# Kernel tuning notes

Measured on AMD Instinct MI355X. Metric: run time of the kernel, lower is better.

The kernel has to match this reference:

```python
import jax, jax.numpy as jnp
import numpy as np

B, TD, TE, H, D, V = 64, 256, 256, 512, 256, 50000

def setup_inputs() -> dict:
    key = jax.random.key(0)
    ks = jax.random.split(key, 8)
    return {
        "enc_outputs": jax.random.normal(ks[0], (B, TE, H), jnp.float32),
        "dec_inputs": jax.random.randint(ks[1], (B, TD), 0, V, jnp.int32),
        "state_h": jax.random.normal(ks[2], (B, H), jnp.float32),
        "state_c": jax.random.normal(ks[3], (B, H), jnp.float32),
        "E": jax.random.normal(ks[4], (V, D), jnp.float32) * 0.02,
        "W": jax.random.normal(ks[5], (D, 4 * H), jnp.float32) * 0.02,
        "U": jax.random.normal(ks[6], (H, 4 * H), jnp.float32) * 0.02,
        "b": jnp.zeros((4 * H,), jnp.float32),
    }


def _masked_lstm(x, mask, h0, c0, W, U, b):
    """Keras-semantics masked LSTM: at masked steps states AND outputs are
    carried from the previous step. Gate order i, f, g(cell), o."""
    def step(carry, inp):
        h, c = carry
        xt, mt = inp  # xt: [B,D], mt: [B]
        z = xt @ W + h @ U + b  # [B,4H]
        i, f, g, o = jnp.split(z, 4, axis=-1)
        c_new = jax.nn.sigmoid(f) * c + jax.nn.sigmoid(i) * jnp.tanh(g)
        h_new = jax.nn.sigmoid(o) * jnp.tanh(c_new)
        m = mt[:, None]
        h2 = jnp.where(m, h_new, h)
        c2 = jnp.where(m, c_new, c)
        return (h2, c2), h2
    xs = (jnp.swapaxes(x, 0, 1), jnp.swapaxes(mask, 0, 1))  # time-major
    (hT, cT), hs = jax.lax.scan(step, (h0, c0), xs)
    return jnp.swapaxes(hs, 0, 1), hT, cT  # [B,Td,H]


def reference(enc_outputs, dec_inputs, state_h, state_c, E, W, U, b):
    mask = dec_inputs != 0  # mask_zero=True on Embedding
    x = E[dec_inputs]  # [B,Td,D]
    dec_outputs, hT, cT = _masked_lstm(x, mask, state_h, state_c, W, U, b)
    # Keras Attention (Luong dot, no scale): query=dec_outputs, key=value=enc_outputs
    scores = jnp.einsum('bqh,bkh->bqk', dec_outputs, enc_outputs)
    probs = jax.nn.softmax(scores, axis=-1)
    ctx = jnp.einsum('bqk,bkh->bqh', probs, enc_outputs)
    # query mask propagated from embedding zeroes masked query rows
    ctx = jnp.where(mask[..., None], ctx, 0.0)
    return (ctx, hT, cT)
```

## Files before the change

### kernel.cpp

```cpp
#include <hip/hip_runtime.h>
#include <stdint.h>

typedef __attribute__((ext_vector_type(4))) float f32x4;
typedef __attribute__((ext_vector_type(4))) int i32x4;
typedef __attribute__((ext_vector_type(4))) unsigned short u16x4;
typedef __attribute__((ext_vector_type(8))) __bf16 bf16x8;

#define NB 64
#define TD 256
#define TE 256
#define HH 512
#define DD 256
#define FH 2048
#define KT 768
#define LDK 776

#define WS_ENC   0u
#define WS_ENCT  16777216u
#define WS_DEC   33554432u
#define WS_HPING 50331648u
#define WS_FLAGS 50462720u
#define WS_WT    50528256u

#define OUT_HT 8388608u
#define OUT_CT 8421376u

__device__ inline unsigned short f2b(float f) {
  union { float f; unsigned u; } x; x.f = f;
  unsigned r = x.u + 0x7FFFu + ((x.u >> 16) & 1u);
  return (unsigned short)(r >> 16);
}
__device__ inline float sigm(float x)   { return 1.0f / (1.0f + __expf(-x)); }
__device__ inline float tanhf_(float x) { return 1.0f - 2.0f / (__expf(2.0f * x) + 1.0f); }

__device__ inline f32x4 mfma_bf16(i32x4 a, i32x4 b, f32x4 c) {
  return __builtin_amdgcn_mfma_f32_16x16x32_bf16(
      __builtin_bit_cast(bf16x8, a), __builtin_bit_cast(bf16x8, b), c, 0, 0, 0);
}

__device__ inline unsigned poll_flag(const unsigned* p) {
  unsigned v;
  asm volatile("global_load_dword %0, %1, off sc0 sc1\n\ts_waitcnt vmcnt(0)"
               : "=v"(v) : "v"(p) : "memory");
  return v;
}
__device__ inline i32x4 load4_bypass(const void* p) {
  i32x4 v;
  asm volatile("global_load_dwordx4 %0, %1, off sc0 sc1" : "=v"(v) : "v"(p) : "memory");
  return v;
}
__device__ inline void store_u16_wt(unsigned short* p, unsigned v) {
  asm volatile("global_store_short %0, %1, off sc0 sc1" :: "v"(p), "v"(v) : "memory");
}
__device__ inline void vm_drain() {
  asm volatile("s_waitcnt vmcnt(0)" ::: "memory");
}
__device__ inline void store_flag(unsigned* p, unsigned v) {
  asm volatile("global_store_dword %0, %1, off sc0 sc1" :: "v"(p), "v"(v) : "memory");
}

__global__ __launch_bounds__(256) void enc_prep(const float* __restrict__ enc,
                                                unsigned short* __restrict__ enc_bf,
                                                unsigned short* __restrict__ encT_bf) {
  __shared__ float tile[64][65];
  const int bid = blockIdx.x;
  const int b  = bid >> 5;
  const int kt = (bid >> 3) & 3;
  const int ht = bid & 7;
  const int tr = threadIdx.x >> 6;
  const int tc = threadIdx.x & 63;
#pragma unroll
  for (int i = 0; i < 16; ++i) {
    const int ke = i * 4 + tr;
    const float v = enc[((size_t)b * TE + kt * 64 + ke) * HH + ht * 64 + tc];
    enc_bf[((size_t)b * TE + kt * 64 + ke) * HH + ht * 64 + tc] = f2b(v);
    tile[ke][tc] = v;
  }
  __syncthreads();
  const int hr4 = threadIdx.x >> 4;
  const int k4  = (threadIdx.x & 15) * 4;
#pragma unroll
  for (int jr = 0; jr < 4; ++jr) {
    const int hr = jr * 16 + hr4;
    u16x4 p = { f2b(tile[k4 + 0][hr]), f2b(tile[k4 + 1][hr]),
                f2b(tile[k4 + 2][hr]), f2b(tile[k4 + 3][hr]) };
    *(u16x4*)&encT_bf[((size_t)b * HH + ht * 64 + hr) * TE + kt * 64 + k4] = p;
  }
}

__global__ __launch_bounds__(256) void w_prep(const float* __restrict__ W,
                                              const float* __restrict__ U,
                                              unsigned short* __restrict__ wT) {
  __shared__ float tile[64][65];
  const int kt = blockIdx.x >> 5;
  const int ct = blockIdx.x & 31;
  const int tr = threadIdx.x >> 6;
  const int tc = threadIdx.x & 63;
#pragma unroll
  for (int i = 0; i < 16; ++i) {
    const int kr = i * 4 + tr;
    const int k  = kt * 64 + kr;
    const float v = (k < DD) ? W[(size_t)k * FH + ct * 64 + tc]
                             : U[(size_t)(k - DD) * FH + ct * 64 + tc];
    tile[kr][tc] = v;
  }
  __syncthreads();
  const int cr4 = threadIdx.x >> 4;
  const int k4  = (threadIdx.x & 15) * 4;
#pragma unroll
  for (int jr = 0; jr < 4; ++jr) {
    const int cr = jr * 16 + cr4;
    u16x4 p = { f2b(tile[k4 + 0][cr]), f2b(tile[k4 + 1][cr]),
                f2b(tile[k4 + 2][cr]), f2b(tile[k4 + 3][cr]) };
    *(u16x4*)&wT[((size_t)ct * 64 + cr) * KT + kt * 64 + k4] = p;
  }
}

__global__ __launch_bounds__(256) void h0_prep(const float* __restrict__ h0,
                                               unsigned short* __restrict__ h_ping,
                                               unsigned* __restrict__ flags) {
  const int i = blockIdx.x * 256 + threadIdx.x;
  if (i < NB * HH) h_ping[i] = f2b(h0[i]);
  if (i < 2 * TD * 32) flags[i] = 0u;
}

__global__ __launch_bounds__(64, 1) void lstm_kernel(
    const float* __restrict__ E, const int* __restrict__ ids,
    const float* __restrict__ h0f, const float* __restrict__ c0f,
    const unsigned short* __restrict__ wT, const float* __restrict__ bias,
    unsigned short* __restrict__ h_ping,
    unsigned short* __restrict__ dec_bf,
    float* __restrict__ out,
    unsigned* __restrict__ flags)
{
  const int lane = threadIdx.x;
  const int g  = blockIdx.x >> 5;
  const int s  = blockIdx.x & 31;
  const int u0 = s << 4;
  const int lhi = lane >> 4;
  const int llo = lane & 15;

  __shared__ __align__(16) unsigned short wt[64 * LDK];
  __shared__ int ids_l[32][260];

  {
    const int r = lane;
    const int c = (r >> 4) * 512 + u0 + (r & 15);
    const unsigned short* src = wT + (size_t)c * KT;
#pragma unroll 8
    for (int j = 0; j < 96; ++j)
      *(i32x4*)&wt[r * LDK + j * 8] = *(const i32x4*)(src + j * 8);
  }
  for (int idx = lane; idx < 32 * 256; idx += 64) {
    const int row = idx >> 8, tt = idx & 255;
    ids_l[row][tt] = ids[(g * 32 + row) * TD + tt];
  }
  __syncthreads();

  float bb[4];
#pragma unroll
  for (int gg = 0; gg < 4; ++gg) bb[gg] = bias[gg * 512 + u0 + llo];

  float h_reg[2][4], c_reg[2][4];
#pragma unroll
  for (int mt = 0; mt < 2; ++mt)
#pragma unroll
    for (int r = 0; r < 4; ++r) {
      const int b = g * 32 + mt * 16 + lhi * 4 + r;
      h_reg[mt][r] = h0f[b * HH + u0 + llo];
      c_reg[mt][r] = c0f[b * HH + u0 + llo];
    }

  unsigned short* hp0 = h_ping;
  unsigned short* hp1 = h_ping + NB * HH;

  for (int t = 0; t < TD; ++t) {
    const unsigned short* h_src = (t & 1) ? hp1 : hp0;
    unsigned short*       h_dst = (t & 1) ? hp0 : hp1;

    int xid[2], mid[2][4];
#pragma unroll
    for (int mt = 0; mt < 2; ++mt) {
      xid[mt] = ids_l[mt * 16 + llo][t];
#pragma unroll
      for (int r = 0; r < 4; ++r) mid[mt][r] = ids_l[mt * 16 + lhi * 4 + r][t];
    }

    i32x4 xf[2][8];
#pragma unroll
    for (int mt = 0; mt < 2; ++mt)
#pragma unroll
      for (int kk = 0; kk < 8; ++kk) {
        const float* ep = E + (size_t)xid[mt] * DD + kk * 32 + lhi * 8;
        f32x4 lo = *(const f32x4*)ep;
        f32x4 hi = *(const f32x4*)(ep + 4);
        union { i32x4 i; unsigned short sh[8]; } u;
        u.sh[0] = f2b(lo[0]); u.sh[1] = f2b(lo[1]); u.sh[2] = f2b(lo[2]); u.sh[3] = f2b(lo[3]);
        u.sh[4] = f2b(hi[0]); u.sh[5] = f2b(hi[1]); u.sh[6] = f2b(hi[2]); u.sh[7] = f2b(hi[3]);
        xf[mt][kk] = u.i;
      }

    f32x4 acc[2][4];
#pragma unroll
    for (int mt = 0; mt < 2; ++mt)
#pragma unroll
      for (int gg = 0; gg < 4; ++gg) acc[mt][gg] = (f32x4){0.f, 0.f, 0.f, 0.f};
#pragma unroll
    for (int kk = 0; kk < 8; ++kk) {
      const int ko = kk * 32 + lhi * 8;
#pragma unroll
      for (int gg = 0; gg < 4; ++gg) {
        i32x4 bfr = *(const i32x4*)&wt[(gg * 16 + llo) * LDK + ko];
        acc[0][gg] = mfma_bf16(xf[0][kk], bfr, acc[0][gg]);
        acc[1][gg] = mfma_bf16(xf[1][kk], bfr, acc[1][gg]);
      }
    }

    if (t > 0) {
      const unsigned* f = flags + ((size_t)g * TD + (t - 1)) * 32;
      for (;;) {
        unsigned v = (lane < 32) ? poll_flag(f + lane) : 1u;
        if (__all(v != 0)) break;
        __builtin_amdgcn_s_sleep(1);
      }
    }

    {
      const unsigned short* hb0 = h_src + (size_t)(g * 32 + llo) * HH + lhi * 8;
      const unsigned short* hb1 = hb0 + 16 * HH;
      i32x4 ha0[16], ha1[16];
#pragma unroll
      for (int kk = 0; kk < 16; ++kk) {
        ha0[kk] = load4_bypass(hb0 + kk * 32);
        ha1[kk] = load4_bypass(hb1 + kk * 32);
      }
      vm_drain();
      __builtin_amdgcn_sched_barrier(0);
#pragma unroll
      for (int kk = 0; kk < 16; ++kk) {
        const int ko = DD + kk * 32 + lhi * 8;
#pragma unroll
        for (int gg = 0; gg < 4; ++gg) {
          i32x4 bfr = *(const i32x4*)&wt[(gg * 16 + llo) * LDK + ko];
          acc[0][gg] = mfma_bf16(ha0[kk], bfr, acc[0][gg]);
          acc[1][gg] = mfma_bf16(ha1[kk], bfr, acc[1][gg]);
        }
      }
    }

    unsigned hb_out[2][4];
#pragma unroll
    for (int mt = 0; mt < 2; ++mt) {
#pragma unroll
      for (int r = 0; r < 4; ++r) {
        const float zi = acc[mt][0][r] + bb[0];
        const float zf = acc[mt][1][r] + bb[1];
        const float zg = acc[mt][2][r] + bb[2];
        const float zo = acc[mt][3][r] + bb[3];
        const float cn = sigm(zf) * c_reg[mt][r] + sigm(zi) * tanhf_(zg);
        const float hn = sigm(zo) * tanhf_(cn);
        if (mid[mt][r] != 0) { c_reg[mt][r] = cn; h_reg[mt][r] = hn; }
        hb_out[mt][r] = f2b(h_reg[mt][r]);
      }
    }

    if (t < TD - 1) {
#pragma unroll
      for (int mt = 0; mt < 2; ++mt)
#pragma unroll
        for (int r = 0; r < 4; ++r) {
          const int b = g * 32 + mt * 16 + lhi * 4 + r;
          store_u16_wt(h_dst + (size_t)b * HH + u0 + llo, hb_out[mt][r]);
        }
      vm_drain();
      if (lane == 0)
        store_flag(flags + ((size_t)g * TD + t) * 32 + s, 1u);
    }

#pragma unroll
    for (int mt = 0; mt < 2; ++mt)
#pragma unroll
      for (int r = 0; r < 4; ++r) {
        const int b = g * 32 + mt * 16 + lhi * 4 + r;
        __builtin_nontemporal_store((unsigned short)hb_out[mt][r],
            &dec_bf[((size_t)b * TD + t) * HH + u0 + llo]);
      }
  }

#pragma unroll
  for (int mt = 0; mt < 2; ++mt)
#pragma unroll
    for (int r = 0; r < 4; ++r) {
      const int b = g * 32 + mt * 16 + lhi * 4 + r;
      out[OUT_HT + (size_t)b * HH + u0 + llo] = h_reg[mt][r];
      out[OUT_CT + (size_t)b * HH + u0 + llo] = c_reg[mt][r];
    }
}

__global__ __launch_bounds__(64, 1) void attn_kernel(
    const unsigned short* __restrict__ dec_bf,
    const unsigned short* __restrict__ enc_bf,
    const unsigned short* __restrict__ encT_bf,
    const int* __restrict__ ids,
    float* __restrict__ out)
{
  const int lane = threadIdx.x;
  const int b  = blockIdx.x >> 4;
  const int q0 = (blockIdx.x & 15) << 4;
  const int lhi = lane >> 4, llo = lane & 15;

  __shared__ __align__(16) unsigned short plds[16 * 264];

  i32x4 qf[16];
  const unsigned short* qb = dec_bf + ((size_t)b * TD + q0 + llo) * HH + lhi * 8;
#pragma unroll
  for (int kk = 0; kk < 16; ++kk) qf[kk] = *(const i32x4*)(qb + kk * 32);

  f32x4 sc[16];
#pragma unroll
  for (int ke = 0; ke < 16; ++ke) sc[ke] = (f32x4){0.f, 0.f, 0.f, 0.f};
#pragma unroll
  for (int kk = 0; kk < 16; ++kk) {
    const unsigned short* eb = enc_bf + ((size_t)b * TE + llo) * HH + kk * 32 + lhi * 8;
#pragma unroll
    for (int ke = 0; ke < 16; ++ke)
      sc[ke] = mfma_bf16(qf[kk], *(const i32x4*)(eb + (size_t)ke * 16 * HH), sc[ke]);
  }

  float mx[4], rinv[4];
#pragma unroll
  for (int r = 0; r < 4; ++r) {
    float m = sc[0][r];
#pragma unroll
    for (int ke = 1; ke < 16; ++ke) m = fmaxf(m, sc[ke][r]);
#pragma unroll
    for (int off = 1; off <= 8; off <<= 1) m = fmaxf(m, __shfl_xor(m, off));
    mx[r] = m;
  }
  float sm[4] = {0.f, 0.f, 0.f, 0.f};
#pragma unroll
  for (int ke = 0; ke < 16; ++ke)
#pragma unroll
    for (int r = 0; r < 4; ++r) {
      const float p = __expf(sc[ke][r] - mx[r]);
      sc[ke][r] = p;
      sm[r] += p;
    }
#pragma unroll
  for (int r = 0; r < 4; ++r) {
    float ss = sm[r];
#pragma unroll
    for (int off = 1; off <= 8; off <<= 1) ss += __shfl_xor(ss, off);
    rinv[r] = 1.0f / ss;
  }

#pragma unroll
  for (int ke = 0; ke < 16; ++ke)
#pragma unroll
    for (int r = 0; r < 4; ++r)
      plds[(lhi * 4 + r) * 264 + ke * 16 + llo] = f2b(sc[ke][r]);
  __syncthreads();

  int mq[4];
#pragma unroll
  for (int r = 0; r < 4; ++r) mq[r] = ids[b * TD + q0 + lhi * 4 + r];

  i32x4 pf[8];
#pragma unroll
  for (int k2 = 0; k2 < 8; ++k2)
    pf[k2] = *(const i32x4*)&plds[llo * 264 + k2 * 32 + lhi * 8];

#pragma unroll
  for (int hh = 0; hh < 2; ++hh) {
    f32x4 cacc[16];
#pragma unroll
    for (int hn = 0; hn < 16; ++hn) cacc[hn] = (f32x4){0.f, 0.f, 0.f, 0.f};
#pragma unroll
    for (int k2 = 0; k2 < 8; ++k2) {
      const unsigned short* tb = encT_bf + ((size_t)b * HH + hh * 256 + llo) * TE + k2 * 32 + lhi * 8;
#pragma unroll
      for (int hn = 0; hn < 16; ++hn)
        cacc[hn] = mfma_bf16(pf[k2], *(const i32x4*)(tb + (size_t)hn * 16 * TE), cacc[hn]);
    }
#pragma unroll
    for (int hn = 0; hn < 16; ++hn)
#pragma unroll
      for (int r = 0; r < 4; ++r) {
        const float vv = mq[r] ? cacc[hn][r] * rinv[r] : 0.0f;
        out[((size_t)b * TD + q0 + lhi * 4 + r) * HH + hh * 256 + hn * 16 + llo] = vv;
      }
  }
}

extern "C" void kernel_launch(void* const* d_in, const int* in_sizes, int n_in,
                              void* d_out, int out_size, void* d_ws, size_t ws_size,
                              hipStream_t stream) {
  const float* enc  = (const float*)d_in[0];
  const int*   ids  = (const int*)d_in[1];
  const float* h0   = (const float*)d_in[2];
  const float* c0   = (const float*)d_in[3];
  const float* E    = (const float*)d_in[4];
  const float* W    = (const float*)d_in[5];
  const float* U    = (const float*)d_in[6];
  const float* bias = (const float*)d_in[7];
  float* out = (float*)d_out;
  char* ws = (char*)d_ws;

  unsigned short* enc_bf  = (unsigned short*)(ws + WS_ENC);
  unsigned short* encT_bf = (unsigned short*)(ws + WS_ENCT);
  unsigned short* dec_bf  = (unsigned short*)(ws + WS_DEC);
  unsigned short* h_ping  = (unsigned short*)(ws + WS_HPING);
  unsigned*       flags   = (unsigned*)(ws + WS_FLAGS);
  unsigned short* wT      = (unsigned short*)(ws + WS_WT);

  enc_prep<<<2048, 256, 0, stream>>>(enc, enc_bf, encT_bf);
  w_prep<<<384, 256, 0, stream>>>(W, U, wT);
  h0_prep<<<128, 256, 0, stream>>>(h0, h_ping, flags);
  lstm_kernel<<<64, 64, 0, stream>>>(E, ids, h0, c0, wT, bias, h_ping, dec_bf, out, flags);
  attn_kernel<<<1024, 64, 0, stream>>>(dec_bf, enc_bf, encT_bf, ids, out);
}
```

Baseline: 1.921 ms.

## Replace per-step flag barrier with timestep-tagged hidden-state words

After: 2.500 ms. +30.1%, slower.

```diff
diff --git a/kernel.cpp b/kernel.cpp
--- a/kernel.cpp
+++ b/kernel.cpp
@@ -18,9 +18,8 @@
 #define WS_ENC   0u
 #define WS_ENCT  16777216u
 #define WS_DEC   33554432u
-#define WS_HPING 50331648u
-#define WS_FLAGS 50462720u
-#define WS_WT    50528256u
+#define WS_HTAG  50331648u
+#define WS_WT    50593792u
 
 #define OUT_HT 8388608u
 #define OUT_CT 8421376u
@@ -38,25 +37,16 @@
       __builtin_bit_cast(bf16x8, a), __builtin_bit_cast(bf16x8, b), c, 0, 0, 0);
 }
 
-__device__ inline unsigned poll_flag(const unsigned* p) {
-  unsigned v;
-  asm volatile("global_load_dword %0, %1, off sc0 sc1\n\ts_waitcnt vmcnt(0)"
-               : "=v"(v) : "v"(p) : "memory");
-  return v;
-}
 __device__ inline i32x4 load4_bypass(const void* p) {
   i32x4 v;
   asm volatile("global_load_dwordx4 %0, %1, off sc0 sc1" : "=v"(v) : "v"(p) : "memory");
   return v;
 }
-__device__ inline void store_u16_wt(unsigned short* p, unsigned v) {
-  asm volatile("global_store_short %0, %1, off sc0 sc1" :: "v"(p), "v"(v) : "memory");
+__device__ inline void store_tag(unsigned* p, unsigned v) {
+  asm volatile("global_store_dword %0, %1, off sc0 sc1" :: "v"(p), "v"(v) : "memory");
 }
 __device__ inline void vm_drain() {
   asm volatile("s_waitcnt vmcnt(0)" ::: "memory");
-}
-__device__ inline void store_flag(unsigned* p, unsigned v) {
-  asm volatile("global_store_dword %0, %1, off sc0 sc1" :: "v"(p), "v"(v) : "memory");
 }
 
 __global__ __launch_bounds__(256) void enc_prep(const float* __restrict__ enc,
@@ -117,21 +107,21 @@
 }
 
 __global__ __launch_bounds__(256) void h0_prep(const float* __restrict__ h0,
-                                               unsigned short* __restrict__ h_ping,
-                                               unsigned* __restrict__ flags) {
+                                               unsigned* __restrict__ htag) {
   const int i = blockIdx.x * 256 + threadIdx.x;
-  if (i < NB * HH) h_ping[i] = f2b(h0[i]);
-  if (i < 2 * TD * 32) flags[i] = 0u;
+  if (i < NB * HH) {
+    htag[i] = (unsigned)f2b(h0[i]);
+    htag[NB * HH + i] = 0u;
+  }
 }
 
 __global__ __launch_bounds__(64, 1) void lstm_kernel(
     const float* __restrict__ E, const int* __restrict__ ids,
     const float* __restrict__ h0f, const float* __restrict__ c0f,
     const unsigned short* __restrict__ wT, const float* __restrict__ bias,
-    unsigned short* __restrict__ h_ping,
+    unsigned* __restrict__ htag,
     unsigned short* __restrict__ dec_bf,
-    float* __restrict__ out,
-    unsigned* __restrict__ flags)
+    float* __restrict__ out)
 {
   const int lane = threadIdx.x;
   const int g  = blockIdx.x >> 5;
@@ -171,12 +161,14 @@
       c_reg[mt][r] = c0f[b * HH + u0 + llo];
     }
 
-  unsigned short* hp0 = h_ping;
-  unsigned short* hp1 = h_ping + NB * HH;
+  unsigned* hbuf0 = htag;
+  unsigned* hbuf1 = htag + NB * HH;
 
   for (int t = 0; t < TD; ++t) {
-    const unsigned short* h_src = (t & 1) ? hp1 : hp0;
-    unsigned short*       h_dst = (t & 1) ? hp0 : hp1;
+    const unsigned* h_src = (t & 1) ? hbuf1 : hbuf0;
+    unsigned*       h_dst = (t & 1) ? hbuf0 : hbuf1;
+    const unsigned  texp  = (unsigned)t;
+    const unsigned  tpub  = (unsigned)(t + 1);
 
     int xid[2], mid[2][4];
 #pragma unroll
@@ -216,41 +208,49 @@
       }
     }
 
-    if (t > 0) {
-      const unsigned* f = flags + ((size_t)g * TD + (t - 1)) * 32;
+#pragma unroll
+    for (int mt = 0; mt < 2; ++mt) {
+      const unsigned* hsrc = h_src + (size_t)(g * 32 + mt * 16 + llo) * HH + lhi * 8;
+      i32x4 ha[16];
       for (;;) {
-        unsigned v = (lane < 32) ? poll_flag(f + lane) : 1u;
-        if (__all(v != 0)) break;
+        i32x4 ra[16], rb[16];
+#pragma unroll
+        for (int kk = 0; kk < 16; ++kk) {
+          ra[kk] = load4_bypass(hsrc + kk * 32);
+          rb[kk] = load4_bypass(hsrc + kk * 32 + 4);
+        }
+        vm_drain();
+        __builtin_amdgcn_sched_barrier(0);
+        unsigned od = 0;
+#pragma unroll
+        for (int kk = 0; kk < 16; ++kk) {
+          od |= (((unsigned)ra[kk][0] >> 16) ^ texp);
+          od |= (((unsigned)rb[kk][0] >> 16) ^ texp);
+        }
+        if (__builtin_expect(__all(od == 0), 1)) {
+#pragma unroll
+          for (int kk = 0; kk < 16; ++kk) {
+            i32x4 f;
+            f[0] = (int)__builtin_amdgcn_perm((unsigned)ra[kk][1], (unsigned)ra[kk][0], 0x05040100u);
+            f[1] = (int)__builtin_amdgcn_perm((unsigned)ra[kk][3], (unsigned)ra[kk][2], 0x05040100u);
+            f[2] = (int)__builtin_amdgcn_perm((unsigned)rb[kk][1], (unsigned)rb[kk][0], 0x05040100u);
+            f[3] = (int)__builtin_amdgcn_perm((unsigned)rb[kk][3], (unsigned)rb[kk][2], 0x05040100u);
+            ha[kk] = f;
+          }
+          break;
+        }
         __builtin_amdgcn_s_sleep(1);
       }
-    }
-
-    {
-      const unsigned short* hb0 = h_src + (size_t)(g * 32 + llo) * HH + lhi * 8;
-      const unsigned short* hb1 = hb0 + 16 * HH;
-      i32x4 ha0[16], ha1[16];
-#pragma unroll
-      for (int kk = 0; kk < 16; ++kk) {
-        ha0[kk] = load4_bypass(hb0 + kk * 32);
-        ha1[kk] = load4_bypass(hb1 + kk * 32);
-      }
-      vm_drain();
-      __builtin_amdgcn_sched_barrier(0);
+
 #pragma unroll
       for (int kk = 0; kk < 16; ++kk) {
         const int ko = DD + kk * 32 + lhi * 8;
 #pragma unroll
-        for (int gg = 0; gg < 4; ++gg) {
-          i32x4 bfr = *(const i32x4*)&wt[(gg * 16 + llo) * LDK + ko];
-          acc[0][gg] = mfma_bf16(ha0[kk], bfr, acc[0][gg]);
-          acc[1][gg] = mfma_bf16(ha1[kk], bfr, acc[1][gg]);
-        }
-      }
-    }
-
-    unsigned hb_out[2][4];
-#pragma unroll
-    for (int mt = 0; mt < 2; ++mt) {
+        for (int gg = 0; gg < 4; ++gg)
+          acc[mt][gg] = mfma_bf16(ha[kk], *(const i32x4*)&wt[(gg * 16 + llo) * LDK + ko],
+                                  acc[mt][gg]);
+      }
+
 #pragma unroll
       for (int r = 0; r < 4; ++r) {
         const float zi = acc[mt][0][r] + bb[0];
@@ -260,31 +260,14 @@
         const float cn = sigm(zf) * c_reg[mt][r] + sigm(zi) * tanhf_(zg);
         const float hn = sigm(zo) * tanhf_(cn);
         if (mid[mt][r] != 0) { c_reg[mt][r] = cn; h_reg[mt][r] = hn; }
-        hb_out[mt][r] = f2b(h_reg[mt][r]);
-      }
-    }
-
-    if (t < TD - 1) {
-#pragma unroll
-      for (int mt = 0; mt < 2; ++mt)
-#pragma unroll
-        for (int r = 0; r < 4; ++r) {
-          const int b = g * 32 + mt * 16 + lhi * 4 + r;
-          store_u16_wt(h_dst + (size_t)b * HH + u0 + llo, hb_out[mt][r]);
-        }
-      vm_drain();
-      if (lane == 0)
-        store_flag(flags + ((size_t)g * TD + t) * 32 + s, 1u);
-    }
-
-#pragma unroll
-    for (int mt = 0; mt < 2; ++mt)
-#pragma unroll
-      for (int r = 0; r < 4; ++r) {
         const int b = g * 32 + mt * 16 + lhi * 4 + r;
-        __builtin_nontemporal_store((unsigned short)hb_out[mt][r],
+        const unsigned hb = f2b(h_reg[mt][r]);
+        if (t < TD - 1)
+          store_tag(h_dst + (size_t)b * HH + u0 + llo, (tpub << 16) | hb);
+        __builtin_nontemporal_store((unsigned short)hb,
             &dec_bf[((size_t)b * TD + t) * HH + u0 + llo]);
       }
+    }
   }
 
 #pragma unroll
@@ -409,13 +392,12 @@
   unsigned short* enc_bf  = (unsigned short*)(ws + WS_ENC);
   unsigned short* encT_bf = (unsigned short*)(ws + WS_ENCT);
   unsigned short* dec_bf  = (unsigned short*)(ws + WS_DEC);
-  unsigned short* h_ping  = (unsigned short*)(ws + WS_HPING);
-  unsigned*       flags   = (unsigned*)(ws + WS_FLAGS);
+  unsigned*       htag    = (unsigned*)(ws + WS_HTAG);
   unsigned short* wT      = (unsigned short*)(ws + WS_WT);
 
   enc_prep<<<2048, 256, 0, stream>>>(enc, enc_bf, encT_bf);
   w_prep<<<384, 256, 0, stream>>>(W, U, wT);
-  h0_prep<<<128, 256, 0, stream>>>(h0, h_ping, flags);
-  lstm_kernel<<<64, 64, 0, stream>>>(E, ids, h0, c0, wT, bias, h_ping, dec_bf, out, flags);
+  h0_prep<<<128, 256, 0, stream>>>(h0, htag);
+  lstm_kernel<<<64, 64, 0, stream>>>(E, ids, h0, c0, wT, bias, htag, dec_bf, out);
   attn_kernel<<<1024, 64, 0, stream>>>(dec_bf, enc_bf, encT_bf, ids, out);
 }
```

## Software-pipeline next-step embedding gather and input GEMM across LSTM steps

Applied to the files above, without the earlier changes.

Result: slower. 2.205 ms (+14.8%).

```diff
diff --git a/kernel.cpp b/kernel.cpp
--- a/kernel.cpp
+++ b/kernel.cpp
@@ -174,24 +174,19 @@
   unsigned short* hp0 = h_ping;
   unsigned short* hp1 = h_ping + NB * HH;
 
-  for (int t = 0; t < TD; ++t) {
-    const unsigned short* h_src = (t & 1) ? hp1 : hp0;
-    unsigned short*       h_dst = (t & 1) ? hp0 : hp1;
-
-    int xid[2], mid[2][4];
+  f32x4 acc[2][4];
+#pragma unroll
+  for (int mt = 0; mt < 2; ++mt)
+#pragma unroll
+    for (int gg = 0; gg < 4; ++gg) acc[mt][gg] = (f32x4){0.f, 0.f, 0.f, 0.f};
+  {
+    i32x4 xf[2][8];
 #pragma unroll
     for (int mt = 0; mt < 2; ++mt) {
-      xid[mt] = ids_l[mt * 16 + llo][t];
-#pragma unroll
-      for (int r = 0; r < 4; ++r) mid[mt][r] = ids_l[mt * 16 + lhi * 4 + r][t];
-    }
-
-    i32x4 xf[2][8];
-#pragma unroll
-    for (int mt = 0; mt < 2; ++mt)
+      const int xid = ids_l[mt * 16 + llo][0];
 #pragma unroll
       for (int kk = 0; kk < 8; ++kk) {
-        const float* ep = E + (size_t)xid[mt] * DD + kk * 32 + lhi * 8;
+        const float* ep = E + (size_t)xid * DD + kk * 32 + lhi * 8;
         f32x4 lo = *(const f32x4*)ep;
         f32x4 hi = *(const f32x4*)(ep + 4);
         union { i32x4 i; unsigned short sh[8]; } u;
@@ -199,12 +194,7 @@
         u.sh[4] = f2b(hi[0]); u.sh[5] = f2b(hi[1]); u.sh[6] = f2b(hi[2]); u.sh[7] = f2b(hi[3]);
         xf[mt][kk] = u.i;
       }
-
-    f32x4 acc[2][4];
-#pragma unroll
-    for (int mt = 0; mt < 2; ++mt)
-#pragma unroll
-      for (int gg = 0; gg < 4; ++gg) acc[mt][gg] = (f32x4){0.f, 0.f, 0.f, 0.f};
+    }
 #pragma unroll
     for (int kk = 0; kk < 8; ++kk) {
       const int ko = kk * 32 + lhi * 8;
@@ -215,36 +205,58 @@
         acc[1][gg] = mfma_bf16(xf[1][kk], bfr, acc[1][gg]);
       }
     }
+  }
+
+  for (int t = 0; t < TD; ++t) {
+    const unsigned short* h_src = (t & 1) ? hp1 : hp0;
+    unsigned short*       h_dst = (t & 1) ? hp0 : hp1;
+
+    int mid[2][4];
+#pragma unroll
+    for (int mt = 0; mt < 2; ++mt)
+#pragma unroll
+      for (int r = 0; r < 4; ++r) mid[mt][r] = ids_l[mt * 16 + lhi * 4 + r][t];
 
     if (t > 0) {
       const unsigned* f = flags + ((size_t)g * TD + (t - 1)) * 32;
       for (;;) {
         unsigned v = (lane < 32) ? poll_flag(f + lane) : 1u;
-        if (__all(v != 0)) break;
+        if (__builtin_expect(__all(v != 0), 1)) break;
         __builtin_amdgcn_s_sleep(1);
       }
     }
 
-    {
-      const unsigned short* hb0 = h_src + (size_t)(g * 32 + llo) * HH + lhi * 8;
-      const unsigned short* hb1 = hb0 + 16 * HH;
-      i32x4 ha0[16], ha1[16];
-#pragma unroll
-      for (int kk = 0; kk < 16; ++kk) {
-        ha0[kk] = load4_bypass(hb0 + kk * 32);
-        ha1[kk] = load4_bypass(hb1 + kk * 32);
-      }
-      vm_drain();
-      __builtin_amdgcn_sched_barrier(0);
-#pragma unroll
-      for (int kk = 0; kk < 16; ++kk) {
-        const int ko = DD + kk * 32 + lhi * 8;
-#pragma unroll
-        for (int gg = 0; gg < 4; ++gg) {
-          i32x4 bfr = *(const i32x4*)&wt[(gg * 16 + llo) * LDK + ko];
-          acc[0][gg] = mfma_bf16(ha0[kk], bfr, acc[0][gg]);
-          acc[1][gg] = mfma_bf16(ha1[kk], bfr, acc[1][gg]);
-        }
+    const unsigned short* hb0 = h_src + (size_t)(g * 32 + llo) * HH + lhi * 8;
+    const unsigned short* hb1 = hb0 + 16 * HH;
+    i32x4 ha0[16], ha1[16];
+#pragma unroll
+    for (int kk = 0; kk < 16; ++kk) {
+      ha0[kk] = load4_bypass(hb0 + kk * 32);
+      ha1[kk] = load4_bypass(hb1 + kk * 32);
+    }
+    const int tn = (t < TD - 1) ? (t + 1) : t;
+    f32x4 xn_lo[2][8], xn_hi[2][8];
+#pragma unroll
+    for (int mt = 0; mt < 2; ++mt) {
+      const int xid = ids_l[mt * 16 + llo][tn];
+#pragma unroll
+      for (int kk = 0; kk < 8; ++kk) {
+        const float* ep = E + (size_t)xid * DD + kk * 32 + lhi * 8;
+        xn_lo[mt][kk] = *(const f32x4*)ep;
+        xn_hi[mt][kk] = *(const f32x4*)(ep + 4);
+      }
+    }
+    vm_drain();
+    __builtin_amdgcn_sched_barrier(0);
+
+#pragma unroll
+    for (int kk = 0; kk < 16; ++kk) {
+      const int ko = DD + kk * 32 + lhi * 8;
+#pragma unroll
+      for (int gg = 0; gg < 4; ++gg) {
+        i32x4 bfr = *(const i32x4*)&wt[(gg * 16 + llo) * LDK + ko];
+        acc[0][gg] = mfma_bf16(ha0[kk], bfr, acc[0][gg]);
+        acc[1][gg] = mfma_bf16(ha1[kk], bfr, acc[1][gg]);
       }
     }
 
@@ -282,9 +294,37 @@
 #pragma unroll
       for (int r = 0; r < 4; ++r) {
         const int b = g * 32 + mt * 16 + lhi * 4 + r;
-        __builtin_nontemporal_store((unsigned short)hb_out[mt][r],
-            &dec_bf[((size_t)b * TD + t) * HH + u0 + llo]);
-      }
+        store_u16_wt(&dec_bf[((size_t)b * TD + t) * HH + u0 + llo], hb_out[mt][r]);
+      }
+
+    if (t < TD - 1) {
+#pragma unroll
+      for (int mt = 0; mt < 2; ++mt)
+#pragma unroll
+        for (int gg = 0; gg < 4; ++gg) acc[mt][gg] = (f32x4){0.f, 0.f, 0.f, 0.f};
+      i32x4 xf[2][8];
+#pragma unroll
+      for (int mt = 0; mt < 2; ++mt)
+#pragma unroll
+        for (int kk = 0; kk < 8; ++kk) {
+          union { i32x4 i; unsigned short sh[8]; } u;
+          u.sh[0] = f2b(xn_lo[mt][kk][0]); u.sh[1] = f2b(xn_lo[mt][kk][1]);
+          u.sh[2] = f2b(xn_lo[mt][kk][2]); u.sh[3] = f2b(xn_lo[mt][kk][3]);
+          u.sh[4] = f2b(xn_hi[mt][kk][0]); u.sh[5] = f2b(xn_hi[mt][kk][1]);
+          u.sh[6] = f2b(xn_hi[mt][kk][2]); u.sh[7] = f2b(xn_hi[mt][kk][3]);
+          xf[mt][kk] = u.i;
+        }
+#pragma unroll
+      for (int kk = 0; kk < 8; ++kk) {
+        const int ko = kk * 32 + lhi * 8;
+#pragma unroll
+        for (int gg = 0; gg < 4; ++gg) {
+          i32x4 bfr = *(const i32x4*)&wt[(gg * 16 + llo) * LDK + ko];
+          acc[0][gg] = mfma_bf16(xf[0][kk], bfr, acc[0][gg]);
+          acc[1][gg] = mfma_bf16(xf[1][kk], bfr, acc[1][gg]);
+        }
+      }
+    }
   }
 
 #pragma unroll
```

## Use atomic counter barrier and vectorized LDS-staged hidden-state stores in LSTM

Applied to the files above, without the earlier changes.

Result: slower. 2.027 ms (+5.5%).

```diff
diff --git a/kernel.cpp b/kernel.cpp
--- a/kernel.cpp
+++ b/kernel.cpp
@@ -19,7 +19,7 @@
 #define WS_ENCT  16777216u
 #define WS_DEC   33554432u
 #define WS_HPING 50331648u
-#define WS_FLAGS 50462720u
+#define WS_CNT   50462720u
 #define WS_WT    50528256u
 
 #define OUT_HT 8388608u
@@ -38,7 +38,7 @@
       __builtin_bit_cast(bf16x8, a), __builtin_bit_cast(bf16x8, b), c, 0, 0, 0);
 }
 
-__device__ inline unsigned poll_flag(const unsigned* p) {
+__device__ inline unsigned poll_word(const unsigned* p) {
   unsigned v;
   asm volatile("global_load_dword %0, %1, off sc0 sc1\n\ts_waitcnt vmcnt(0)"
                : "=v"(v) : "v"(p) : "memory");
@@ -49,14 +49,14 @@
   asm volatile("global_load_dwordx4 %0, %1, off sc0 sc1" : "=v"(v) : "v"(p) : "memory");
   return v;
 }
-__device__ inline void store_u16_wt(unsigned short* p, unsigned v) {
-  asm volatile("global_store_short %0, %1, off sc0 sc1" :: "v"(p), "v"(v) : "memory");
+__device__ inline void store4_wt(void* p, i32x4 v) {
+  asm volatile("global_store_dwordx4 %0, %1, off sc0 sc1" :: "v"(p), "v"(v) : "memory");
 }
 __device__ inline void vm_drain() {
   asm volatile("s_waitcnt vmcnt(0)" ::: "memory");
 }
-__device__ inline void store_flag(unsigned* p, unsigned v) {
-  asm volatile("global_store_dword %0, %1, off sc0 sc1" :: "v"(p), "v"(v) : "memory");
+__device__ inline void lds_fence() {
+  asm volatile("s_waitcnt lgkmcnt(0)" ::: "memory");
 }
 
 __global__ __launch_bounds__(256) void enc_prep(const float* __restrict__ enc,
@@ -118,10 +118,10 @@
 
 __global__ __launch_bounds__(256) void h0_prep(const float* __restrict__ h0,
                                                unsigned short* __restrict__ h_ping,
-                                               unsigned* __restrict__ flags) {
+                                               unsigned* __restrict__ cnt) {
   const int i = blockIdx.x * 256 + threadIdx.x;
   if (i < NB * HH) h_ping[i] = f2b(h0[i]);
-  if (i < 2 * TD * 32) flags[i] = 0u;
+  if (i < 2 * TD) cnt[i] = 0u;
 }
 
 __global__ __launch_bounds__(64, 1) void lstm_kernel(
@@ -131,7 +131,7 @@
     unsigned short* __restrict__ h_ping,
     unsigned short* __restrict__ dec_bf,
     float* __restrict__ out,
-    unsigned* __restrict__ flags)
+    unsigned* __restrict__ cnt)
 {
   const int lane = threadIdx.x;
   const int g  = blockIdx.x >> 5;
@@ -142,6 +142,7 @@
 
   __shared__ __align__(16) unsigned short wt[64 * LDK];
   __shared__ int ids_l[32][260];
+  __shared__ __align__(64) unsigned short hT[32][32];
 
   {
     const int r = lane;
@@ -217,10 +218,10 @@
     }
 
     if (t > 0) {
-      const unsigned* f = flags + ((size_t)g * TD + (t - 1)) * 32;
+      const unsigned* c = cnt + (size_t)g * TD + (t - 1);
       for (;;) {
-        unsigned v = (lane < 32) ? poll_flag(f + lane) : 1u;
-        if (__all(v != 0)) break;
+        unsigned v = poll_word(c);
+        if (__builtin_expect(v >= 32u, 1)) break;
         __builtin_amdgcn_s_sleep(1);
       }
     }
@@ -260,21 +261,23 @@
         const float cn = sigm(zf) * c_reg[mt][r] + sigm(zi) * tanhf_(zg);
         const float hn = sigm(zo) * tanhf_(cn);
         if (mid[mt][r] != 0) { c_reg[mt][r] = cn; h_reg[mt][r] = hn; }
-        hb_out[mt][r] = f2b(h_reg[mt][r]);
+        const unsigned hb = f2b(h_reg[mt][r]);
+        hb_out[mt][r] = hb;
+        hT[mt * 16 + lhi * 4 + r][llo] = (unsigned short)hb;
       }
     }
 
     if (t < TD - 1) {
-#pragma unroll
-      for (int mt = 0; mt < 2; ++mt)
-#pragma unroll
-        for (int r = 0; r < 4; ++r) {
-          const int b = g * 32 + mt * 16 + lhi * 4 + r;
-          store_u16_wt(h_dst + (size_t)b * HH + u0 + llo, hb_out[mt][r]);
-        }
+      lds_fence();
+      __builtin_amdgcn_sched_barrier(0);
+      const int br = lane >> 1;
+      const int half = lane & 1;
+      i32x4 hv = *(const i32x4*)&hT[br][half * 8];
+      store4_wt(h_dst + (size_t)(g * 32 + br) * HH + u0 + half * 8, hv);
       vm_drain();
       if (lane == 0)
-        store_flag(flags + ((size_t)g * TD + t) * 32 + s, 1u);
+        __hip_atomic_fetch_add(cnt + (size_t)g * TD + t, 1u,
+                               __ATOMIC_RELEASE, __HIP_MEMORY_SCOPE_AGENT);
     }
 
 #pragma unroll
@@ -410,12 +413,12 @@
   unsigned short* encT_bf = (unsigned short*)(ws + WS_ENCT);
   unsigned short* dec_bf  = (unsigned short*)(ws + WS_DEC);
   unsigned short* h_ping  = (unsigned short*)(ws + WS_HPING);
-  unsigned*       flags   = (unsigned*)(ws + WS_FLAGS);
+  unsigned*       cnt     = (unsigned*)(ws + WS_CNT);
   unsigned short* wT      = (unsigned short*)(ws + WS_WT);
 
   enc_prep<<<2048, 256, 0, stream>>>(enc, enc_bf, encT_bf);
   w_prep<<<384, 256, 0, stream>>>(W, U, wT);
-  h0_prep<<<128, 256, 0, stream>>>(h0, h_ping, flags);
-  lstm_kernel<<<64, 64, 0, stream>>>(E, ids, h0, c0, wT, bias, h_ping, dec_bf, out, flags);
+  h0_prep<<<128, 256, 0, stream>>>(h0, h_ping, cnt);
+  lstm_kernel<<<64, 64, 0, stream>>>(E, ids, h0, c0, wT, bias, h_ping, dec_bf, out, cnt);
   attn_kernel<<<1024, 64, 0, stream>>>(dec_bf, enc_bf, encT_bf, ids, out);
 }
```
